# Performance work log

Hardware: AMD Instinct MI355X
Metric: run time of the kernel (lower is better)

Reference implementation:

```python
import jax, jax.numpy as jnp
import numpy as np

V, E, H, C = 50000, 300, 512, 3
B, P_LEN, H_LEN = 64, 128, 64


def _lstm(x, Wih, Whh, bih, bhh, h0, c0):
    """torch-style LSTM (gate order i,f,g,o). x: [B,T,E] -> outputs [B,T,H], hT, cT."""
    def step(carry, xt):
        h, c = carry
        g = xt @ Wih.T + h @ Whh.T + bih + bhh  # [B,4H]
        i, f, gg, o = jnp.split(g, 4, axis=-1)
        c = jax.nn.sigmoid(f) * c + jax.nn.sigmoid(i) * jnp.tanh(gg)
        h = jax.nn.sigmoid(o) * jnp.tanh(c)
        return (h, c), h
    (hT, cT), ys = jax.lax.scan(step, (h0, c0), jnp.swapaxes(x, 0, 1))
    return jnp.swapaxes(ys, 0, 1), hT, cT


def setup_inputs() -> dict:
    key = jax.random.key(0)
    ks = iter(jax.random.split(key, 32))
    n = lambda shape, s=0.05: jax.random.normal(next(ks), shape, dtype=jnp.float32) * s
    inp = {
        "premise": jax.random.randint(next(ks), (B, P_LEN), 0, V, dtype=jnp.int32),
        "hypothesis": jax.random.randint(next(ks), (B, H_LEN), 0, V, dtype=jnp.int32),
        "emb": n((V, E), 0.1),
        "Wih1": n((4 * H, E)), "Whh1": n((4 * H, H)), "bih1": n((4 * H,)), "bhh1": n((4 * H,)),
        "Wih2": n((4 * H, E)), "Whh2": n((4 * H, H)), "bih2": n((4 * H,)), "bhh2": n((4 * H,)),
        "W_y": n((H, H)), "W_h": n((H, H)), "W_r": n((H, H)), "W_t": n((H, H)),
        "w_att": n((1, H)),
        "fc1_w": n((H, H)), "fc1_b": n((H,)),
        "fc2_w": n((H, H)), "fc2_b": n((H,)),
        "fc3_w": n((C, H)), "fc3_b": n((C,)),
    }
    return inp


def reference(premise, hypothesis, emb,
              Wih1, Whh1, bih1, bhh1,
              Wih2, Whh2, bih2, bhh2,
              W_y, W_h, W_r, W_t, w_att,
              fc1_w, fc1_b, fc2_w, fc2_b, fc3_w, fc3_b):
    Bsz = premise.shape[0]
    Hd = Whh1.shape[1]
    zeros = jnp.zeros((Bsz, Hd), jnp.float32)

    # premise LSTM
    xp = emb[premise]                                   # [B,P,E]
    out_p, _, c_p = _lstm(xp, Wih1, Whh1, bih1, bhh1, zeros, zeros)
    # hypothesis LSTM initialized with (h0=0, c0=c_p)
    xh = emb[hypothesis]                                # [B,Th,E]
    out_h, hn_h, _ = _lstm(xh, Wih2, Whh2, bih2, bhh2, zeros, c_p)

    # word-by-word attention: a1 = W_y @ V^T, fixed across steps
    a1 = jnp.einsum('hj,bpj->bhp', W_y, out_p)          # [B,H,P]
    wv = w_att[0]                                       # [H]

    def att_step(r, q_t):
        # r: [B,H] attention state; q_t: [B,H] hypothesis step
        a2 = q_t @ W_h.T + r @ W_r.T                    # [B,H]
        s = jnp.einsum('h,bhp->bp', wv, jnp.tanh(a1 + a2[:, :, None]))
        scores = jax.nn.softmax(s, axis=-1)             # over premise positions
        r = jnp.einsum('bph,bp->bh', out_p, scores) + jnp.tanh(r @ W_t.T)
        return r, None

    r, _ = jax.lax.scan(att_step, zeros, jnp.swapaxes(out_h, 0, 1))

    rep = jnp.tanh(r @ fc1_w.T + fc1_b + hn_h @ fc2_w.T + fc2_b)
    return rep @ fc3_w.T + fc3_b                         # [B,C]
```

## Files before the change

### kernel.cpp

```cpp
#include <hip/hip_runtime.h>
#include <math.h>

#define BSZ 64
#define PLEN 128
#define HLEN 64
#define EDIM 300
#define HDIM 512
#define G4 2048
#define NCLS 3

#define TOFF 1000u
#define SPIN_CAP (1 << 18)

#define CHROW 528
#define CH(f) ((((f) >> 7) * 132) + ((f) & 127))

__device__ __forceinline__ float sigf(float x) { return 1.0f / (1.0f + __expf(-x)); }
__device__ __forceinline__ float tanhfast(float x) { return 1.0f - 2.0f / (__expf(2.0f * x) + 1.0f); }

__device__ __forceinline__ unsigned long long aload64(const unsigned long long* p) {
    return __hip_atomic_load(p, __ATOMIC_RELAXED, __HIP_MEMORY_SCOPE_AGENT);
}
__device__ __forceinline__ void astore64(unsigned long long* p, unsigned long long v) {
    __hip_atomic_store(p, v, __ATOMIC_RELAXED, __HIP_MEMORY_SCOPE_AGENT);
}
__device__ __forceinline__ unsigned long long tpack(float v, unsigned tag) {
    return ((unsigned long long)tag << 32) | (unsigned long long)__float_as_uint(v);
}
__device__ __forceinline__ float tval(unsigned long long v) { return __uint_as_float((unsigned)v); }
__device__ __forceinline__ unsigned ttag(unsigned long long v) { return (unsigned)(v >> 32); }

__global__ __launch_bounds__(256) void ws_zero(unsigned long long* p) {
    p[(size_t)blockIdx.x * 256 + threadIdx.x] = 0ull;
}

__global__ __launch_bounds__(256) void proj_kernel(
    const int* __restrict__ toks, const float* __restrict__ emb,
    const float* __restrict__ Wih, const float* __restrict__ bih,
    const float* __restrict__ bhh, float* __restrict__ out)
{
    __shared__ float es[32 * 100];
    __shared__ float wsh[64 * 100];
    __shared__ int tks[32];
    const int m0 = blockIdx.x * 32, r0 = blockIdx.y * 64;
    const int tid = threadIdx.x;
    const int tx = tid & 15, ty = tid >> 4;
    float acc[2][4] = {{0.f, 0.f, 0.f, 0.f}, {0.f, 0.f, 0.f, 0.f}};
    if (tid < 32) tks[tid] = toks[m0 + tid];
    __syncthreads();
    for (int kc = 0; kc < 3; kc++) {
        if (kc) __syncthreads();
        for (int i = tid; i < 800; i += 256) {
            int row = i / 25, k4 = i % 25;
            ((float4*)es)[i] = ((const float4*)(emb + (size_t)tks[row] * EDIM + kc * 100))[k4];
        }
        for (int i = tid; i < 1600; i += 256) {
            int row = i / 25, k4 = i % 25;
            ((float4*)wsh)[i] = ((const float4*)(Wih + (size_t)(r0 + row) * EDIM + kc * 100))[k4];
        }
        __syncthreads();
        const float4* e0 = (const float4*)es + ty * 25;
        const float4* e1 = e0 + 16 * 25;
        const float4* w0 = (const float4*)wsh + tx * 25;
#pragma unroll
        for (int k = 0; k < 25; k++) {
            float4 ea = e0[k], eb = e1[k];
#pragma unroll
            for (int j = 0; j < 4; j++) {
                float4 w = w0[k + j * 400];
                acc[0][j] += ea.x * w.x + ea.y * w.y + ea.z * w.z + ea.w * w.w;
                acc[1][j] += eb.x * w.x + eb.y * w.y + eb.z * w.z + eb.w * w.w;
            }
        }
    }
#pragma unroll
    for (int j = 0; j < 4; j++) {
        int rr = r0 + tx + j * 16;
        float bsum = bih[rr] + bhh[rr];
        out[(size_t)(m0 + ty) * G4 + rr]      = acc[0][j] + bsum;
        out[(size_t)(m0 + ty + 16) * G4 + rr] = acc[1][j] + bsum;
    }
}

__global__ __launch_bounds__(256, 1) void lstm_coop(
    const float* __restrict__ xp, const float* __restrict__ xh,
    const float* __restrict__ Whh1, const float* __restrict__ Whh2,
    float* __restrict__ outp, float* __restrict__ outh,
    unsigned long long* __restrict__ hA, unsigned long long* __restrict__ hB,
    unsigned long long* __restrict__ hC, unsigned long long* __restrict__ hD)
{
    const int tid = threadIdx.x;
    const int ug = blockIdx.x & 31;
    const int bg = blockIdx.x >> 5;
    const int u0 = ug * 16, b0 = bg * 8;
    const int r = tid >> 2, c = tid & 3;
    const int g = r >> 4, uur = r & 15;

    __shared__ __align__(16) float hst[8 * CHROW];
    __shared__ float gsm[64][9];

    float4 w[32];
    {
        const float4* src = (const float4*)(Whh1 + ((size_t)(g * HDIM + u0 + uur)) * HDIM) + c * 32;
#pragma unroll
        for (int k = 0; k < 32; k++) w[k] = src[k];
    }
    float creg = 0.0f;
    const int bbc = tid >> 4, uuc = tid & 15;

    for (int t = 0; t < PLEN + HLEN; t++) {
        const int layer2 = (t >= PLEN) ? 1 : 0;
        const int tloc = layer2 ? t - PLEN : t;
        const int T = layer2 ? HLEN : PLEN;
        const float* xproj = layer2 ? xh : xp;
        float* outseq = layer2 ? outh : outp;
        unsigned long long* wA = layer2 ? hC : hA;
        unsigned long long* wB = layer2 ? hD : hB;
        unsigned long long* hwr = (t & 1) ? wB : wA;
        const unsigned long long* hrd = (t & 1) ? wA : wB;

        float gi = 0.f, gf = 0.f, gg = 0.f, go = 0.f;
        if (tid < 128) {
            size_t xb = ((size_t)(b0 + bbc) * T + tloc) * G4 + u0 + uuc;
            gi = xproj[xb];        gf = xproj[xb + 512];
            gg = xproj[xb + 1024]; go = xproj[xb + 1536];
        }

        if (t == PLEN) {
            const float4* src = (const float4*)(Whh2 + ((size_t)(g * HDIM + u0 + uur)) * HDIM) + c * 32;
#pragma unroll
            for (int k = 0; k < 32; k++) w[k] = src[k];
        }
        const bool have_h = (tloc != 0);
        if (have_h) {
            const unsigned long long* src = hrd + (size_t)b0 * 512;
            unsigned long long v[16];
            const unsigned expt = (unsigned)t;
            int guard = 0;
            while (true) {
                bool ok = true;
#pragma unroll
                for (int i = 0; i < 16; i++) v[i] = aload64(src + tid + i * 256);
#pragma unroll
                for (int i = 0; i < 16; i++) ok &= (ttag(v[i]) == expt);
                if (__all(ok)) break;
                if (++guard > SPIN_CAP) break;
                __builtin_amdgcn_s_sleep(1);
            }
            __asm__ volatile("" ::: "memory");
#pragma unroll
            for (int i = 0; i < 16; i++) {
                int idx = tid + i * 256;
                int bb = idx >> 9, u = idx & 511;
                hst[bb * CHROW + CH(u)] = tval(v[i]);
            }
            __syncthreads();
#pragma unroll 1
            for (int bb = 0; bb < 8; bb++) {
                const float4* hv = (const float4*)&hst[bb * CHROW + c * 132];
                float ax = 0.f, ay = 0.f, az = 0.f, aw = 0.f;
#pragma unroll
                for (int k = 0; k < 32; k++) {
                    float4 a = w[k], x = hv[k];
                    ax += a.x * x.x; ay += a.y * x.y; az += a.z * x.z; aw += a.w * x.w;
                }
                float acc = (ax + ay) + (az + aw);
                acc += __shfl_xor(acc, 1);
                acc += __shfl_xor(acc, 2);
                if (c == 0) gsm[r][bb] = acc;
            }
        }
        __syncthreads();
        if (tid < 128) {
            const int b = b0 + bbc;
            if (have_h) {
                gi += gsm[uuc][bbc];
                gf += gsm[16 + uuc][bbc];
                gg += gsm[32 + uuc][bbc];
                go += gsm[48 + uuc][bbc];
            }
            float cn = sigf(gf) * creg + sigf(gi) * tanhfast(gg);
            float hn = sigf(go) * tanhfast(cn);
            creg = cn;
            astore64(hwr + (size_t)b * 512 + u0 + uuc, tpack(hn, (unsigned)(t + 1)));
            outseq[((size_t)b * T + tloc) * HDIM + u0 + uuc] = hn;
        }
    }
}

__global__ __launch_bounds__(256) void a1_kernel(
    const float* __restrict__ Wy, const float* __restrict__ outp,
    float* __restrict__ a1t)
{
    __shared__ float os[32 * 132];
    __shared__ float wsh[64 * 132];
    const int b = blockIdx.x, p0 = blockIdx.y * 32, h0 = blockIdx.z * 64;
    const int tid = threadIdx.x;
    const int tx = tid & 15, ty = tid >> 4;
    float acc[2][4] = {{0.f, 0.f, 0.f, 0.f}, {0.f, 0.f, 0.f, 0.f}};
    for (int kc = 0; kc < 4; kc++) {
        if (kc) __syncthreads();
        for (int i = tid; i < 1024; i += 256) {
            int row = i >> 5, k4 = i & 31;
            ((float4*)os)[row * 33 + k4] =
                ((const float4*)(outp + ((size_t)(b * PLEN) + p0 + row) * HDIM + kc * 128))[k4];
        }
        for (int i = tid; i < 2048; i += 256) {
            int row = i >> 5, k4 = i & 31;
            ((float4*)wsh)[row * 33 + k4] =
                ((const float4*)(Wy + (size_t)(h0 + row) * HDIM + kc * 128))[k4];
        }
        __syncthreads();
        const float4* o0 = (const float4*)os + ty * 33;
        const float4* o1 = o0 + 16 * 33;
        const float4* w0 = (const float4*)wsh + tx * 33;
#pragma unroll
        for (int k = 0; k < 32; k++) {
            float4 ea = o0[k], eb = o1[k];
#pragma unroll
            for (int j = 0; j < 4; j++) {
                float4 w = w0[k + j * 528];
                acc[0][j] += ea.x * w.x + ea.y * w.y + ea.z * w.z + ea.w * w.w;
                acc[1][j] += eb.x * w.x + eb.y * w.y + eb.z * w.z + eb.w * w.w;
            }
        }
    }
#pragma unroll
    for (int j = 0; j < 4; j++) {
        int hh = h0 + tx + j * 16;
        a1t[((size_t)b * PLEN + p0 + ty) * HDIM + hh]      = acc[0][j];
        a1t[((size_t)b * PLEN + p0 + ty + 16) * HDIM + hh] = acc[1][j];
    }
}

#define OSTR 2056
__global__ __launch_bounds__(256, 1) void att_coop(
    const float* __restrict__ outh, const float* __restrict__ a1b,
    const float* __restrict__ outp,
    const float* __restrict__ Wh, const float* __restrict__ Wr,
    const float* __restrict__ Wt, const float* __restrict__ wv,
    unsigned long long* __restrict__ a2buf, unsigned long long* __restrict__ sbuf,
    unsigned long long* __restrict__ rA, unsigned long long* __restrict__ rB)
{
    const int tid = threadIdx.x;
    const int ug = blockIdx.x & 31;
    const int bg = blockIdx.x >> 5;
    const int u0 = ug * 16, b0 = bg * 8;
    const int r = tid >> 2, c = tid & 3;
    const int m = r >> 4, uur = r & 15;

    __shared__ __align__(16) float ops[8 * OSTR];
    __shared__ __align__(16) float qa[8 * CHROW];
    __shared__ __align__(16) float rst[8 * CHROW];
    __shared__ __align__(16) float scst[8][132];
    __shared__ float dsm[48][9];
    __shared__ float tts[16][9];
    __shared__ __align__(16) float wvs[512];

    float4 w[32];
    if (r < 48) {
        const float* W = (m == 0) ? Wh : ((m == 1) ? Wr : Wt);
        const float4* src = (const float4*)(W + (size_t)(u0 + uur) * HDIM) + c * 32;
#pragma unroll
        for (int k = 0; k < 32; k++) w[k] = src[k];
    }
    for (int i = tid; i < 128; i += 256)
        ((float4*)wvs)[i] = ((const float4*)wv)[i];

    for (int i = tid; i < 8 * 128 * 4; i += 256) {
        int bb = i >> 9;
        int rem = i & 511;
        int p = rem >> 2, q = rem & 3;
        float4 v = *((const float4*)(outp + ((size_t)(b0 + bb) * PLEN + p) * HDIM + u0) + q);
        *((float4*)(ops + bb * OSTR + p * 16) + q) = v;
    }

    const int wvid = tid >> 6, lane = tid & 63;
    const int p0g = ug * 4;
    float4 a1r[8][2];
#pragma unroll
    for (int i = 0; i < 8; i++) {
        int pr = wvid * 8 + i;
        int bb = pr >> 2, pp = pr & 3;
        const float4* src = (const float4*)(a1b + ((size_t)(b0 + bb) * PLEN + p0g + pp) * HDIM) + lane;
        a1r[i][0] = src[0];
        a1r[i][1] = src[64];
    }

    const int bbc = tid >> 4, uuc = tid & 15;

    for (int t = 0; t < HLEN; t++) {
        unsigned long long* rwr = (t & 1) ? rB : rA;
        const unsigned long long* rrd = (t & 1) ? rA : rB;

        for (int i = tid; i < 8 * 128; i += 256) {
            int bb = i >> 7, k4 = i & 127;
            float4 v = ((const float4*)(outh + ((size_t)(b0 + bb) * HLEN + t) * HDIM))[k4];
            *(float4*)&qa[bb * CHROW + CH(4 * k4)] = v;
        }
        if (t > 0) {
            const unsigned long long* src = rrd + (size_t)b0 * 512;
            unsigned long long v[16];
            const unsigned expt = TOFF + (unsigned)(3 * t);
            int guard = 0;
            while (true) {
                bool ok = true;
#pragma unroll
                for (int i = 0; i < 16; i++) v[i] = aload64(src + tid + i * 256);
#pragma unroll
                for (int i = 0; i < 16; i++) ok &= (ttag(v[i]) == expt);
                if (__all(ok)) break;
                if (++guard > SPIN_CAP) break;
                __builtin_amdgcn_s_sleep(1);
            }
            __asm__ volatile("" ::: "memory");
#pragma unroll
            for (int i = 0; i < 16; i++) {
                int idx = tid + i * 256;
                int bb = idx >> 9, u = idx & 511;
                rst[bb * CHROW + CH(u)] = tval(v[i]);
            }
        }
        __syncthreads();
        if (r < 48 && (t > 0 || m == 0)) {
#pragma unroll 1
            for (int bb = 0; bb < 8; bb++) {
                const float4* sv = (const float4*)((m == 0) ? &qa[bb * CHROW + c * 132]
                                                            : &rst[bb * CHROW + c * 132]);
                float ax = 0.f, ay = 0.f, az = 0.f, aw = 0.f;
#pragma unroll
                for (int k = 0; k < 32; k++) {
                    float4 a = w[k], x = sv[k];
                    ax += a.x * x.x; ay += a.y * x.y; az += a.z * x.z; aw += a.w * x.w;
                }
                float acc = (ax + ay) + (az + aw);
                acc += __shfl_xor(acc, 1);
                acc += __shfl_xor(acc, 2);
                if (c == 0) dsm[r][bb] = acc;
            }
        }
        __syncthreads();
        if (tid < 128) {
            float aq = dsm[uuc][bbc];
            float ar = (t > 0) ? dsm[16 + uuc][bbc] : 0.0f;
            float at = (t > 0) ? dsm[32 + uuc][bbc] : 0.0f;
            float a2v = aq + ar;
            tts[uuc][bbc] = (t > 0) ? tanhfast(at) : 0.0f;
            astore64(a2buf + (size_t)(b0 + bbc) * 512 + u0 + uuc,
                     tpack(a2v, TOFF + (unsigned)(3 * t + 1)));
        }

        {
            const unsigned long long* src = a2buf + (size_t)b0 * 512;
            unsigned long long v[16];
            const unsigned expt = TOFF + (unsigned)(3 * t + 1);
            int guard = 0;
            while (true) {
                bool ok = true;
#pragma unroll
                for (int i = 0; i < 16; i++) v[i] = aload64(src + tid + i * 256);
#pragma unroll
                for (int i = 0; i < 16; i++) ok &= (ttag(v[i]) == expt);
                if (__all(ok)) break;
                if (++guard > SPIN_CAP) break;
                __builtin_amdgcn_s_sleep(1);
            }
            __asm__ volatile("" ::: "memory");
#pragma unroll
            for (int i = 0; i < 16; i++) {
                int idx = tid + i * 256;
                int bb = idx >> 9, u = idx & 511;
                qa[bb * CHROW + CH(u)] = tval(v[i]);
            }
        }
        __syncthreads();
        {
#pragma unroll 2
            for (int i = 0; i < 8; i++) {
                int pr = wvid * 8 + i;
                int bb = pr >> 2, pp = pr & 3;
                float s = 0.f;
#pragma unroll
                for (int k = 0; k < 2; k++) {
                    int h4 = lane + 64 * k;
                    float4 av = a1r[i][k];
                    float4 a2v = *(const float4*)&qa[bb * CHROW + CH(4 * h4)];
                    float4 wv4 = ((const float4*)wvs)[h4];
                    s += wv4.x * tanhfast(av.x + a2v.x)
                       + wv4.y * tanhfast(av.y + a2v.y)
                       + wv4.z * tanhfast(av.z + a2v.z)
                       + wv4.w * tanhfast(av.w + a2v.w);
                }
#pragma unroll
                for (int o = 1; o < 64; o <<= 1) s += __shfl_xor(s, o);
                if (lane == 0)
                    astore64(sbuf + (size_t)(b0 + bb) * PLEN + p0g + pp,
                             tpack(s, TOFF + (unsigned)(3 * t + 2)));
            }
        }

        {
            const unsigned long long* src = sbuf + (size_t)b0 * 128;
            unsigned long long v[4];
            const unsigned expt = TOFF + (unsigned)(3 * t + 2);
            int guard = 0;
            while (true) {
                bool ok = true;
#pragma unroll
                for (int i = 0; i < 4; i++) v[i] = aload64(src + tid + i * 256);
#pragma unroll
                for (int i = 0; i < 4; i++) ok &= (ttag(v[i]) == expt);
                if (__all(ok)) break;
                if (++guard > SPIN_CAP) break;
                __builtin_amdgcn_s_sleep(1);
            }
            __asm__ volatile("" ::: "memory");
#pragma unroll
            for (int i = 0; i < 4; i++) {
                int idx = tid + i * 256;
                int bb = idx >> 7, j = idx & 127;
                scst[bb][j] = tval(v[i]);
            }
        }
        __syncthreads();
        {
            const int bb = tid >> 5, j = tid & 31;
            float4 v = *(float4*)&scst[bb][j * 4];
            float mx = fmaxf(fmaxf(v.x, v.y), fmaxf(v.z, v.w));
#pragma unroll
            for (int o = 1; o < 32; o <<= 1) mx = fmaxf(mx, __shfl_xor(mx, o));
            float ex = __expf(v.x - mx), ey = __expf(v.y - mx);
            float ez = __expf(v.z - mx), ew = __expf(v.w - mx);
            float ssum = (ex + ey) + (ez + ew);
#pragma unroll
            for (int o = 1; o < 32; o <<= 1) ssum += __shfl_xor(ssum, o);
            float inv = 1.0f / ssum;
            float4 sc4 = make_float4(ex * inv, ey * inv, ez * inv, ew * inv);
            *(float4*)&scst[bb][j * 4] = sc4;
        }
        __syncthreads();
        if (tid < 128) {
            float acc = tts[uuc][bbc];
            const float* opb = ops + bbc * OSTR + uuc;
#pragma unroll 8
            for (int p = 0; p < PLEN; p++)
                acc += scst[bbc][p] * opb[p * 16];
            astore64(rwr + (size_t)(b0 + bbc) * 512 + u0 + uuc,
                     tpack(acc, TOFF + (unsigned)(3 * t + 3)));
        }
    }
}

__global__ __launch_bounds__(256) void final_kernel(
    const unsigned long long* __restrict__ r2, const float* __restrict__ outh,
    const float* __restrict__ fc1w, const float* __restrict__ fc1b,
    const float* __restrict__ fc2w, const float* __restrict__ fc2b,
    const float* __restrict__ fc3w, const float* __restrict__ fc3b,
    float* __restrict__ out)
{
    int b = blockIdx.x, tid = threadIdx.x;
    __shared__ float rs[HDIM], hs[HDIM], rep[HDIM], red[256];
    for (int i = tid; i < 512; i += 256)
        rs[i] = tval(r2[(size_t)b * 512 + i]);
    for (int i = tid; i < 128; i += 256)
        ((float4*)hs)[i] = ((const float4*)(outh + ((size_t)(b * HLEN + HLEN - 1)) * HDIM))[i];
    __syncthreads();
    for (int u = tid; u < HDIM; u += 256) {
        const float4* w1 = (const float4*)(fc1w + (size_t)u * HDIM);
        const float4* w2 = (const float4*)(fc2w + (size_t)u * HDIM);
        float a = 0.f, bacc = 0.f;
        for (int k = 0; k < 128; k++) {
            float4 rv = ((float4*)rs)[k], hv = ((float4*)hs)[k];
            float4 x = w1[k]; a    += rv.x * x.x + rv.y * x.y + rv.z * x.z + rv.w * x.w;
            float4 y = w2[k]; bacc += hv.x * y.x + hv.y * y.y + hv.z * y.z + hv.w * y.w;
        }
        rep[u] = tanhfast(a + fc1b[u] + bacc + fc2b[u]);
    }
    __syncthreads();
    for (int cix = 0; cix < NCLS; cix++) {
        red[tid] = rep[tid] * fc3w[(size_t)cix * HDIM + tid]
                 + rep[tid + 256] * fc3w[(size_t)cix * HDIM + tid + 256];
        __syncthreads();
        for (int off = 128; off; off >>= 1) {
            if (tid < off) red[tid] += red[tid + off];
            __syncthreads();
        }
        if (tid == 0) out[b * NCLS + cix] = red[0] + fc3b[cix];
        __syncthreads();
    }
}

extern "C" void kernel_launch(void* const* d_in, const int* in_sizes, int n_in,
                              void* d_out, int out_size, void* d_ws, size_t ws_size,
                              hipStream_t stream)
{
    const int*   premise = (const int*)d_in[0];
    const int*   hyp     = (const int*)d_in[1];
    const float* emb     = (const float*)d_in[2];
    const float* Wih1    = (const float*)d_in[3];
    const float* Whh1    = (const float*)d_in[4];
    const float* bih1    = (const float*)d_in[5];
    const float* bhh1    = (const float*)d_in[6];
    const float* Wih2    = (const float*)d_in[7];
    const float* Whh2    = (const float*)d_in[8];
    const float* bih2    = (const float*)d_in[9];
    const float* bhh2    = (const float*)d_in[10];
    const float* Wy      = (const float*)d_in[11];
    const float* Wh      = (const float*)d_in[12];
    const float* Wr      = (const float*)d_in[13];
    const float* Wt      = (const float*)d_in[14];
    const float* wv      = (const float*)d_in[15];
    const float* fc1w    = (const float*)d_in[16];
    const float* fc1b    = (const float*)d_in[17];
    const float* fc2w    = (const float*)d_in[18];
    const float* fc2b    = (const float*)d_in[19];
    const float* fc3w    = (const float*)d_in[20];
    const float* fc3b    = (const float*)d_in[21];
    float* out = (float*)d_out;

    float* ws = (float*)d_ws;
    size_t off = 0;
    float* xp    = ws + off; off += (size_t)BSZ * PLEN * G4;
    float* xh    = ws + off; off += (size_t)BSZ * HLEN * G4;
    float* outp  = ws + off; off += (size_t)BSZ * PLEN * HDIM;
    float* outhp = ws + off; off += (size_t)BSZ * HLEN * HDIM;
    float* a1b   = ws + off; off += (size_t)BSZ * HDIM * PLEN;
    unsigned long long* tbase = (unsigned long long*)(ws + off);
    unsigned long long* hAb   = tbase;
    unsigned long long* hBb   = tbase + 32768;
    unsigned long long* a2buf = tbase + 2 * 32768;
    unsigned long long* rAb   = tbase + 3 * 32768;
    unsigned long long* rBb   = tbase + 4 * 32768;
    unsigned long long* sbuf  = tbase + 5 * 32768;
    off += (size_t)(5 * 32768 + 8192) * 2;
    if (ws_size < off * sizeof(float)) return;

    ws_zero<<<dim3(672), dim3(256), 0, stream>>>(tbase);

    proj_kernel<<<dim3(BSZ * PLEN / 32, G4 / 64), dim3(256), 0, stream>>>(
        premise, emb, Wih1, bih1, bhh1, xp);
    proj_kernel<<<dim3(BSZ * HLEN / 32, G4 / 64), dim3(256), 0, stream>>>(
        hyp, emb, Wih2, bih2, bhh2, xh);

    lstm_coop<<<dim3(256), dim3(256), 0, stream>>>(
        xp, xh, Whh1, Whh2, outp, outhp, hAb, hBb, rAb, rBb);

    a1_kernel<<<dim3(BSZ, PLEN / 32, HDIM / 64), dim3(256), 0, stream>>>(Wy, outp, a1b);

    att_coop<<<dim3(256), dim3(256), 0, stream>>>(
        outhp, a1b, outp, Wh, Wr, Wt, wv, a2buf, sbuf, rAb, rBb);

    final_kernel<<<dim3(BSZ), dim3(256), 0, stream>>>(
        rBb, outhp, fc1w, fc1b, fc2w, fc2b, fc3w, fc3b, out);
}
```

Measured before the change: 3.664 ms.

## Fuse input projection into persistent LSTM kernel with prefetched embeddings

Removes the separate proj_kernel launches and the large xp/xh gate buffers. Each persistent LSTM block keeps its slice of Wih in shared memory, prefetches the next step's embedding rows into a double buffer, and computes the input projection inside the recurrence while waiting for h. The spin-wait loops also change to load every value once and then reload only the entries whose tags are stale. In exchange, each serial step does extra work and uses more shared memory.

```diff
diff --git a/kernel.cpp b/kernel.cpp
--- a/kernel.cpp
+++ b/kernel.cpp
@@ -34,57 +34,13 @@
     p[(size_t)blockIdx.x * 256 + threadIdx.x] = 0ull;
 }
 
-__global__ __launch_bounds__(256) void proj_kernel(
-    const int* __restrict__ toks, const float* __restrict__ emb,
-    const float* __restrict__ Wih, const float* __restrict__ bih,
-    const float* __restrict__ bhh, float* __restrict__ out)
-{
-    __shared__ float es[32 * 100];
-    __shared__ float wsh[64 * 100];
-    __shared__ int tks[32];
-    const int m0 = blockIdx.x * 32, r0 = blockIdx.y * 64;
-    const int tid = threadIdx.x;
-    const int tx = tid & 15, ty = tid >> 4;
-    float acc[2][4] = {{0.f, 0.f, 0.f, 0.f}, {0.f, 0.f, 0.f, 0.f}};
-    if (tid < 32) tks[tid] = toks[m0 + tid];
-    __syncthreads();
-    for (int kc = 0; kc < 3; kc++) {
-        if (kc) __syncthreads();
-        for (int i = tid; i < 800; i += 256) {
-            int row = i / 25, k4 = i % 25;
-            ((float4*)es)[i] = ((const float4*)(emb + (size_t)tks[row] * EDIM + kc * 100))[k4];
-        }
-        for (int i = tid; i < 1600; i += 256) {
-            int row = i / 25, k4 = i % 25;
-            ((float4*)wsh)[i] = ((const float4*)(Wih + (size_t)(r0 + row) * EDIM + kc * 100))[k4];
-        }
-        __syncthreads();
-        const float4* e0 = (const float4*)es + ty * 25;
-        const float4* e1 = e0 + 16 * 25;
-        const float4* w0 = (const float4*)wsh + tx * 25;
-#pragma unroll
-        for (int k = 0; k < 25; k++) {
-            float4 ea = e0[k], eb = e1[k];
-#pragma unroll
-            for (int j = 0; j < 4; j++) {
-                float4 w = w0[k + j * 400];
-                acc[0][j] += ea.x * w.x + ea.y * w.y + ea.z * w.z + ea.w * w.w;
-                acc[1][j] += eb.x * w.x + eb.y * w.y + eb.z * w.z + eb.w * w.w;
-            }
-        }
-    }
-#pragma unroll
-    for (int j = 0; j < 4; j++) {
-        int rr = r0 + tx + j * 16;
-        float bsum = bih[rr] + bhh[rr];
-        out[(size_t)(m0 + ty) * G4 + rr]      = acc[0][j] + bsum;
-        out[(size_t)(m0 + ty + 16) * G4 + rr] = acc[1][j] + bsum;
-    }
-}
-
 __global__ __launch_bounds__(256, 1) void lstm_coop(
-    const float* __restrict__ xp, const float* __restrict__ xh,
-    const float* __restrict__ Whh1, const float* __restrict__ Whh2,
+    const int* __restrict__ premise, const int* __restrict__ hyp,
+    const float* __restrict__ emb,
+    const float* __restrict__ Wih1, const float* __restrict__ bih1,
+    const float* __restrict__ bhh1, const float* __restrict__ Whh1,
+    const float* __restrict__ Wih2, const float* __restrict__ bih2,
+    const float* __restrict__ bhh2, const float* __restrict__ Whh2,
     float* __restrict__ outp, float* __restrict__ outh,
     unsigned long long* __restrict__ hA, unsigned long long* __restrict__ hB,
     unsigned long long* __restrict__ hC, unsigned long long* __restrict__ hD)
@@ -96,15 +52,46 @@
     const int r = tid >> 2, c = tid & 3;
     const int g = r >> 4, uur = r & 15;
 
+    __shared__ __align__(16) float wih[64 * 304];
+    __shared__ __align__(16) float ebuf[2][8 * 304];
     __shared__ __align__(16) float hst[8 * CHROW];
     __shared__ float gsm[64][9];
-
+    __shared__ float bs[128];
+    __shared__ int tkl[8 * 192];
+
+    for (int i = tid; i < 8 * 192; i += 256) {
+        int bb = i / 192, tt = i % 192;
+        tkl[i] = (tt < PLEN) ? premise[(b0 + bb) * PLEN + tt]
+                             : hyp[(b0 + bb) * HLEN + (tt - PLEN)];
+    }
+    for (int i = tid; i < 64 * 76; i += 256) {
+        int row = i / 76, f4 = i % 76;
+        int grow = (row >> 4) * HDIM + u0 + (row & 15);
+        float4 v = (f4 < 75) ? ((const float4*)(Wih1 + (size_t)grow * EDIM))[f4]
+                             : make_float4(0.f, 0.f, 0.f, 0.f);
+        *((float4*)&wih[row * 304] + f4) = v;
+    }
+    if (tid < 64) {
+        int grow = (tid >> 4) * HDIM + u0 + (tid & 15);
+        bs[tid]      = bih1[grow] + bhh1[grow];
+        bs[64 + tid] = bih2[grow] + bhh2[grow];
+    }
     float4 w[32];
     {
         const float4* src = (const float4*)(Whh1 + ((size_t)(g * HDIM + u0 + uur)) * HDIM) + c * 32;
 #pragma unroll
         for (int k = 0; k < 32; k++) w[k] = src[k];
     }
+    __syncthreads();
+    for (int i = tid; i < 608; i += 256) {
+        int bb = i / 76, f4 = i % 76;
+        int tok = tkl[bb * 192];
+        float4 v = (f4 < 75) ? ((const float4*)(emb + (size_t)tok * EDIM))[f4]
+                             : make_float4(0.f, 0.f, 0.f, 0.f);
+        *((float4*)&ebuf[0][bb * 304] + f4) = v;
+    }
+    __syncthreads();
+
     float creg = 0.0f;
     const int bbc = tid >> 4, uuc = tid & 15;
 
@@ -112,51 +99,104 @@
         const int layer2 = (t >= PLEN) ? 1 : 0;
         const int tloc = layer2 ? t - PLEN : t;
         const int T = layer2 ? HLEN : PLEN;
-        const float* xproj = layer2 ? xh : xp;
         float* outseq = layer2 ? outh : outp;
         unsigned long long* wA = layer2 ? hC : hA;
         unsigned long long* wB = layer2 ? hD : hB;
         unsigned long long* hwr = (t & 1) ? wB : wA;
         const unsigned long long* hrd = (t & 1) ? wA : wB;
 
-        float gi = 0.f, gf = 0.f, gg = 0.f, go = 0.f;
-        if (tid < 128) {
-            size_t xb = ((size_t)(b0 + bbc) * T + tloc) * G4 + u0 + uuc;
-            gi = xproj[xb];        gf = xproj[xb + 512];
-            gg = xproj[xb + 1024]; go = xproj[xb + 1536];
+        float4 pf0 = make_float4(0.f, 0.f, 0.f, 0.f);
+        float4 pf1 = pf0, pf2 = pf0;
+        const bool havepf = (t + 1 < PLEN + HLEN);
+        const int i2 = tid + 512;
+        if (havepf) {
+            {   int bb = tid / 76, f4 = tid % 76;
+                int tok = tkl[bb * 192 + t + 1];
+                if (f4 < 75) pf0 = ((const float4*)(emb + (size_t)tok * EDIM))[f4]; }
+            {   int i1 = tid + 256; int bb = i1 / 76, f4 = i1 % 76;
+                int tok = tkl[bb * 192 + t + 1];
+                if (f4 < 75) pf1 = ((const float4*)(emb + (size_t)tok * EDIM))[f4]; }
+            if (i2 < 608) {
+                int bb = i2 / 76, f4 = i2 % 76;
+                int tok = tkl[bb * 192 + t + 1];
+                if (f4 < 75) pf2 = ((const float4*)(emb + (size_t)tok * EDIM))[f4]; }
         }
 
         if (t == PLEN) {
             const float4* src = (const float4*)(Whh2 + ((size_t)(g * HDIM + u0 + uur)) * HDIM) + c * 32;
 #pragma unroll
             for (int k = 0; k < 32; k++) w[k] = src[k];
-        }
+            for (int i = tid; i < 64 * 76; i += 256) {
+                int row = i / 76, f4 = i % 76;
+                int grow = (row >> 4) * HDIM + u0 + (row & 15);
+                float4 v = (f4 < 75) ? ((const float4*)(Wih2 + (size_t)grow * EDIM))[f4]
+                                     : make_float4(0.f, 0.f, 0.f, 0.f);
+                *((float4*)&wih[row * 304] + f4) = v;
+            }
+            __syncthreads();
+        }
+
+        float xacc[8];
+#pragma unroll
+        for (int bb = 0; bb < 8; bb++) xacc[bb] = 0.f;
+        {
+            const float4* wx = (const float4*)&wih[r * 304] + c * 19;
+            const float* ebp = &ebuf[t & 1][0];
+#pragma unroll
+            for (int k = 0; k < 19; k++) {
+                float4 wv4 = wx[k];
+#pragma unroll
+                for (int bb = 0; bb < 8; bb++) {
+                    float4 ev = *((const float4*)&ebp[bb * 304] + c * 19 + k);
+                    xacc[bb] += wv4.x * ev.x + wv4.y * ev.y + wv4.z * ev.z + wv4.w * ev.w;
+                }
+            }
+        }
+
         const bool have_h = (tloc != 0);
+        unsigned long long v[16];
         if (have_h) {
             const unsigned long long* src = hrd + (size_t)b0 * 512;
-            unsigned long long v[16];
             const unsigned expt = (unsigned)t;
+#pragma unroll
+            for (int i = 0; i < 16; i++) v[i] = aload64(src + tid + i * 256);
             int guard = 0;
             while (true) {
                 bool ok = true;
-#pragma unroll
-                for (int i = 0; i < 16; i++) v[i] = aload64(src + tid + i * 256);
 #pragma unroll
                 for (int i = 0; i < 16; i++) ok &= (ttag(v[i]) == expt);
                 if (__all(ok)) break;
                 if (++guard > SPIN_CAP) break;
                 __builtin_amdgcn_s_sleep(1);
+#pragma unroll
+                for (int i = 0; i < 16; i++)
+                    if (ttag(v[i]) != expt) v[i] = aload64(src + tid + i * 256);
             }
             __asm__ volatile("" ::: "memory");
+        }
+
+        if (have_h) {
 #pragma unroll
             for (int i = 0; i < 16; i++) {
                 int idx = tid + i * 256;
                 int bb = idx >> 9, u = idx & 511;
                 hst[bb * CHROW + CH(u)] = tval(v[i]);
             }
-            __syncthreads();
+        }
+        if (havepf) {
+            float* ep = &ebuf[(t + 1) & 1][0];
+            *((float4*)&ep[(tid / 76) * 304] + (tid % 76)) = pf0;
+            {   int i1 = tid + 256;
+                *((float4*)&ep[(i1 / 76) * 304] + (i1 % 76)) = pf1; }
+            if (i2 < 608)
+                *((float4*)&ep[(i2 / 76) * 304] + (i2 % 76)) = pf2;
+        }
+        __syncthreads();
+
 #pragma unroll 1
-            for (int bb = 0; bb < 8; bb++) {
+        for (int bb = 0; bb < 8; bb++) {
+            float acc;
+            if (have_h) {
                 const float4* hv = (const float4*)&hst[bb * CHROW + c * 132];
                 float ax = 0.f, ay = 0.f, az = 0.f, aw = 0.f;
 #pragma unroll
@@ -164,21 +204,23 @@
                     float4 a = w[k], x = hv[k];
                     ax += a.x * x.x; ay += a.y * x.y; az += a.z * x.z; aw += a.w * x.w;
                 }
-                float acc = (ax + ay) + (az + aw);
-                acc += __shfl_xor(acc, 1);
-                acc += __shfl_xor(acc, 2);
-                if (c == 0) gsm[r][bb] = acc;
-            }
-        }
-        __syncthreads();
+                acc = (ax + ay) + (az + aw) + xacc[bb];
+            } else {
+                acc = xacc[bb];
+            }
+            acc += __shfl_xor(acc, 1);
+            acc += __shfl_xor(acc, 2);
+            if (c == 0) gsm[r][bb] = acc;
+        }
+        __syncthreads();
+
         if (tid < 128) {
             const int b = b0 + bbc;
-            if (have_h) {
-                gi += gsm[uuc][bbc];
-                gf += gsm[16 + uuc][bbc];
-                gg += gsm[32 + uuc][bbc];
-                go += gsm[48 + uuc][bbc];
-            }
+            const float* bsl = &bs[layer2 * 64];
+            float gi = gsm[uuc][bbc]      + bsl[uuc];
+            float gf = gsm[16 + uuc][bbc] + bsl[16 + uuc];
+            float gg = gsm[32 + uuc][bbc] + bsl[32 + uuc];
+            float go = gsm[48 + uuc][bbc] + bsl[48 + uuc];
             float cn = sigf(gf) * creg + sigf(gi) * tanhfast(gg);
             float hn = sigf(go) * tanhfast(cn);
             creg = cn;
@@ -302,16 +344,19 @@
             const unsigned long long* src = rrd + (size_t)b0 * 512;
             unsigned long long v[16];
             const unsigned expt = TOFF + (unsigned)(3 * t);
+#pragma unroll
+            for (int i = 0; i < 16; i++) v[i] = aload64(src + tid + i * 256);
             int guard = 0;
             while (true) {
                 bool ok = true;
-#pragma unroll
-                for (int i = 0; i < 16; i++) v[i] = aload64(src + tid + i * 256);
 #pragma unroll
                 for (int i = 0; i < 16; i++) ok &= (ttag(v[i]) == expt);
                 if (__all(ok)) break;
                 if (++guard > SPIN_CAP) break;
                 __builtin_amdgcn_s_sleep(1);
+#pragma unroll
+                for (int i = 0; i < 16; i++)
+                    if (ttag(v[i]) != expt) v[i] = aload64(src + tid + i * 256);
             }
             __asm__ volatile("" ::: "memory");
 #pragma unroll
@@ -354,16 +399,19 @@
             const unsigned long long* src = a2buf + (size_t)b0 * 512;
             unsigned long long v[16];
             const unsigned expt = TOFF + (unsigned)(3 * t + 1);
+#pragma unroll
+            for (int i = 0; i < 16; i++) v[i] = aload64(src + tid + i * 256);
             int guard = 0;
             while (true) {
                 bool ok = true;
-#pragma unroll
-                for (int i = 0; i < 16; i++) v[i] = aload64(src + tid + i * 256);
 #pragma unroll
                 for (int i = 0; i < 16; i++) ok &= (ttag(v[i]) == expt);
                 if (__all(ok)) break;
                 if (++guard > SPIN_CAP) break;
                 __builtin_amdgcn_s_sleep(1);
+#pragma unroll
+                for (int i = 0; i < 16; i++)
+                    if (ttag(v[i]) != expt) v[i] = aload64(src + tid + i * 256);
             }
             __asm__ volatile("" ::: "memory");
 #pragma unroll
@@ -403,16 +451,19 @@
             const unsigned long long* src = sbuf + (size_t)b0 * 128;
             unsigned long long v[4];
             const unsigned expt = TOFF + (unsigned)(3 * t + 2);
+#pragma unroll
+            for (int i = 0; i < 4; i++) v[i] = aload64(src + tid + i * 256);
             int guard = 0;
             while (true) {
                 bool ok = true;
-#pragma unroll
-                for (int i = 0; i < 4; i++) v[i] = aload64(src + tid + i * 256);
 #pragma unroll
                 for (int i = 0; i < 4; i++) ok &= (ttag(v[i]) == expt);
                 if (__all(ok)) break;
                 if (++guard > SPIN_CAP) break;
                 __builtin_amdgcn_s_sleep(1);
+#pragma unroll
+                for (int i = 0; i < 4; i++)
+                    if (ttag(v[i]) != expt) v[i] = aload64(src + tid + i * 256);
             }
             __asm__ volatile("" ::: "memory");
 #pragma unroll
@@ -520,8 +571,6 @@
 
     float* ws = (float*)d_ws;
     size_t off = 0;
-    float* xp    = ws + off; off += (size_t)BSZ * PLEN * G4;
-    float* xh    = ws + off; off += (size_t)BSZ * HLEN * G4;
     float* outp  = ws + off; off += (size_t)BSZ * PLEN * HDIM;
     float* outhp = ws + off; off += (size_t)BSZ * HLEN * HDIM;
     float* a1b   = ws + off; off += (size_t)BSZ * HDIM * PLEN;
@@ -537,13 +586,11 @@
 
     ws_zero<<<dim3(672), dim3(256), 0, stream>>>(tbase);
 
-    proj_kernel<<<dim3(BSZ * PLEN / 32, G4 / 64), dim3(256), 0, stream>>>(
-        premise, emb, Wih1, bih1, bhh1, xp);
-    proj_kernel<<<dim3(BSZ * HLEN / 32, G4 / 64), dim3(256), 0, stream>>>(
-        hyp, emb, Wih2, bih2, bhh2, xh);
-
     lstm_coop<<<dim3(256), dim3(256), 0, stream>>>(
-        xp, xh, Whh1, Whh2, outp, outhp, hAb, hBb, rAb, rBb);
+        premise, hyp, emb,
+        Wih1, bih1, bhh1, Whh1,
+        Wih2, bih2, bhh2, Whh2,
+        outp, outhp, hAb, hBb, rAb, rBb);
 
     a1_kernel<<<dim3(BSZ, PLEN / 32, HDIM / 64), dim3(256), 0, stream>>>(Wy, outp, a1b);
 
```

New measurement: 12.35 ms. 3.37x slower.
